# Kernel tuning notes

Hardware: AMD Instinct MI355X
Metric: run time of the kernel (lower is better)

## Reference

```python
import jax, jax.numpy as jnp
import numpy as np


def setup_inputs() -> dict:
    key = jax.random.key(0)
    B, H = 4096, 32768
    x = jax.random.normal(key, (B, H), dtype=jnp.float32)
    return {"hidden_preactivation_BH": x, "k": 64}


def reference(hidden_preactivation_BH, k):
    # top-k over last dim, then scatter values back into a zero tensor
    vals_BK, idx_BK = jax.lax.top_k(hidden_preactivation_BH, k)
    B = hidden_preactivation_BH.shape[0]
    rows_B1 = jnp.arange(B)[:, None]
    hidden_BH = jnp.zeros_like(hidden_preactivation_BH)
    hidden_BH = hidden_BH.at[rows_B1, idx_BK].set(vals_BK)
    return hidden_BH
```

## Files before the change

### kernel.cpp

```cpp
#include <hip/hip_runtime.h>
#include <stdint.h>


#define H_DIM    32768
#define NTHREADS 1024
#define VPT      (H_DIM / NTHREADS / 4)
#define CAP      2048
#define NBINS    4096

__device__ __forceinline__ uint32_t f2mono(float f) {
    uint32_t u = __float_as_uint(f);
    return (u & 0x80000000u) ? ~u : (u | 0x80000000u);
}
__device__ __forceinline__ float mono2f(uint32_t m) {
    uint32_t u = (m & 0x80000000u) ? (m & 0x7fffffffu) : ~m;
    return __uint_as_float(u);
}

__global__ __launch_bounds__(NTHREADS)
void topk_kernel(const float* __restrict__ in, const int* __restrict__ kp,
                 float* __restrict__ out)
{
    __shared__ uint32_t hist[NBINS];
    __shared__ uint32_t wave_exc[16];
    __shared__ uint32_t s_b, s_g, s_cnt;
    __shared__ uint32_t s_ncand;
    __shared__ uint32_t cand_u[CAP];
    __shared__ uint32_t cand_i[CAP];

    const uint32_t t   = threadIdx.x;
    const uint32_t row = blockIdx.x;
    const uint32_t k   = (uint32_t)kp[0];

    const float4* __restrict__ rin  = (const float4*)(in  + (size_t)row * H_DIM);
    float4*       __restrict__ rout = (float4*)(out + (size_t)row * H_DIM);

    #pragma unroll
    for (int i = 0; i < NBINS / NTHREADS; ++i) hist[t + i * NTHREADS] = 0;
    if (t == 0) s_ncand = 0;
    __syncthreads();

    uint32_t um[VPT][4];
    #pragma unroll
    for (int it = 0; it < VPT; ++it) {
        float4 v = rin[t + it * NTHREADS];
        um[it][0] = f2mono(v.x);
        um[it][1] = f2mono(v.y);
        um[it][2] = f2mono(v.z);
        um[it][3] = f2mono(v.w);
        atomicAdd(&hist[um[it][0] >> 20], 1u);
        atomicAdd(&hist[um[it][1] >> 20], 1u);
        atomicAdd(&hist[um[it][2] >> 20], 1u);
        atomicAdd(&hist[um[it][3] >> 20], 1u);
    }
    __syncthreads();

    {
        uint32_t h0 = hist[4*t], h1 = hist[4*t+1], h2 = hist[4*t+2], h3 = hist[4*t+3];
        uint32_t s = h0 + h1 + h2 + h3;
        uint32_t lane = t & 63, wid = t >> 6;
        uint32_t v = s;
        #pragma unroll
        for (int off = 1; off < 64; off <<= 1) {
            uint32_t o = __shfl_down(v, off);
            if (lane + off < 64) v += o;
        }
        if (lane == 0) wave_exc[wid] = v;
        __syncthreads();
        if (t == 0) {
            uint32_t acc = 0;
            for (int w = 15; w >= 0; --w) { uint32_t tw = wave_exc[w]; wave_exc[w] = acc; acc += tw; }
        }
        __syncthreads();
        uint32_t cumIncl = v + wave_exc[wid];
        uint32_t Ech = cumIncl - s;
        if (Ech < k && k <= Ech + s) {
            uint32_t gl = Ech;
            #pragma unroll
            for (int bb = 3; bb >= 0; --bb) {
                uint32_t h = hist[4*t + bb];
                if (gl + h >= k) { s_b = 4*t + (uint32_t)bb; s_g = gl; s_cnt = h; break; }
                gl += h;
            }
        }
    }
    __syncthreads();

    uint32_t prefix = s_b;
    uint32_t g      = s_g;
    uint32_t cnt    = s_cnt;
    uint32_t shift  = 20;

    while (cnt > CAP && shift > 0) {
        uint32_t nshift = (shift >= 12) ? (shift - 12) : 0;
        uint32_t nbits  = shift - nshift;
        uint32_t nbins  = 1u << nbits;
        __syncthreads();
        for (uint32_t i = t; i < nbins; i += NTHREADS) hist[i] = 0;
        __syncthreads();
        #pragma unroll
        for (int it = 0; it < VPT; ++it) {
            #pragma unroll
            for (int c = 0; c < 4; ++c) {
                uint32_t u = um[it][c];
                if ((u >> shift) == prefix)
                    atomicAdd(&hist[(u >> nshift) & (nbins - 1)], 1u);
            }
        }
        __syncthreads();
        if (t == 0) {
            uint32_t gl = g;
            for (int bb = (int)nbins - 1; bb >= 0; --bb) {
                uint32_t h = hist[bb];
                if (gl + h >= k) { s_b = (uint32_t)bb; s_g = gl; s_cnt = h; break; }
                gl += h;
            }
        }
        __syncthreads();
        prefix = (prefix << nbits) | s_b;
        g = s_g; cnt = s_cnt; shift = nshift;
    }

    const uint32_t need = k - g;
    #pragma unroll
    for (int it = 0; it < VPT; ++it) {
        float4 o;
        float* oc = (float*)&o;
        #pragma unroll
        for (int c = 0; c < 4; ++c) {
            uint32_t u  = um[it][c];
            uint32_t hi = u >> shift;
            float val = 0.0f;
            if (hi > prefix) {
                val = mono2f(u);
            } else if (hi == prefix) {
                uint32_t p = atomicAdd(&s_ncand, 1u);
                if (p < CAP) { cand_u[p] = u; cand_i[p] = (t + (uint32_t)it * NTHREADS) * 4u + (uint32_t)c; }
            }
            oc[c] = val;
        }
        rout[t + it * NTHREADS] = o;
    }
    __syncthreads();

    uint32_t nc = s_ncand; if (nc > CAP) nc = CAP;
    for (uint32_t i = t; i < nc; i += NTHREADS) {
        uint32_t ui = cand_u[i], ii = cand_i[i];
        uint32_t rank = 0;
        for (uint32_t j = 0; j < nc; ++j) {
            uint32_t uj = cand_u[j];
            rank += (uj > ui || (uj == ui && cand_i[j] < ii)) ? 1u : 0u;
        }
        if (rank < need) out[(size_t)row * H_DIM + ii] = mono2f(ui);
    }
}

extern "C" void kernel_launch(void* const* d_in, const int* in_sizes, int n_in,
                              void* d_out, int out_size, void* d_ws, size_t ws_size,
                              hipStream_t stream)
{
    const float* x  = (const float*)d_in[0];
    const int*   kp = (const int*)d_in[1];
    float* out = (float*)d_out;
    const int B = in_sizes[0] / H_DIM;
    hipLaunchKernelGGL(topk_kernel, dim3(B), dim3(NTHREADS), 0, stream, x, kp, out);
}
```

Baseline: 232.9 us.

## Use persistent blocks with next-row prefetch, bitmap candidate select, nontemporal IO

Launches a fixed grid of 256 persistent blocks that loop over rows, prefetching the next row into registers while the current row is processed. Selected boundary candidates are recorded in a shared bitmap so the output is written once with coalesced nontemporal stores, replacing scattered single-element writes after the main store. It also adds raw s_barrier sync and nontemporal loads. The cost is higher register pressure from the prefetch buffer, and a 256-block grid may underfill the GPU compared with one block per row.

```diff
diff --git a/kernel.cpp b/kernel.cpp
--- a/kernel.cpp
+++ b/kernel.cpp
@@ -7,6 +7,9 @@
 #define VPT      (H_DIM / NTHREADS / 4)
 #define CAP      2048
 #define NBINS    4096
+#define NWORDS   (H_DIM / 32)
+
+typedef float f32x4 __attribute__((ext_vector_type(4)));
 
 __device__ __forceinline__ uint32_t f2mono(float f) {
     uint32_t u = __float_as_uint(f);
@@ -17,141 +20,190 @@
     return __uint_as_float(u);
 }
 
-__global__ __launch_bounds__(NTHREADS)
+__device__ __forceinline__ void BAR() {
+    asm volatile("s_waitcnt lgkmcnt(0)" ::: "memory");
+    __builtin_amdgcn_s_barrier();
+}
+
+__global__ __launch_bounds__(NTHREADS, 4)
 void topk_kernel(const float* __restrict__ in, const int* __restrict__ kp,
-                 float* __restrict__ out)
+                 float* __restrict__ out, int B)
 {
     __shared__ uint32_t hist[NBINS];
+    __shared__ uint32_t bitmap[NWORDS];
     __shared__ uint32_t wave_exc[16];
     __shared__ uint32_t s_b, s_g, s_cnt;
     __shared__ uint32_t s_ncand;
     __shared__ uint32_t cand_u[CAP];
     __shared__ uint32_t cand_i[CAP];
 
-    const uint32_t t   = threadIdx.x;
-    const uint32_t row = blockIdx.x;
-    const uint32_t k   = (uint32_t)kp[0];
-
-    const float4* __restrict__ rin  = (const float4*)(in  + (size_t)row * H_DIM);
-    float4*       __restrict__ rout = (float4*)(out + (size_t)row * H_DIM);
-
-    #pragma unroll
-    for (int i = 0; i < NBINS / NTHREADS; ++i) hist[t + i * NTHREADS] = 0;
-    if (t == 0) s_ncand = 0;
-    __syncthreads();
-
-    uint32_t um[VPT][4];
-    #pragma unroll
-    for (int it = 0; it < VPT; ++it) {
-        float4 v = rin[t + it * NTHREADS];
-        um[it][0] = f2mono(v.x);
-        um[it][1] = f2mono(v.y);
-        um[it][2] = f2mono(v.z);
-        um[it][3] = f2mono(v.w);
-        atomicAdd(&hist[um[it][0] >> 20], 1u);
-        atomicAdd(&hist[um[it][1] >> 20], 1u);
-        atomicAdd(&hist[um[it][2] >> 20], 1u);
-        atomicAdd(&hist[um[it][3] >> 20], 1u);
+    const uint32_t t = threadIdx.x;
+    const uint32_t k = (uint32_t)kp[0];
+
+    int row = (int)blockIdx.x;
+    const int rstride = (int)gridDim.x;
+
+    f32x4 buf[VPT];
+    if (row < B) {
+        const f32x4* __restrict__ rin = (const f32x4*)(in + (size_t)row * H_DIM);
+        #pragma unroll
+        for (int i = 0; i < VPT; ++i)
+            buf[i] = __builtin_nontemporal_load(&rin[t + i * NTHREADS]);
     }
-    __syncthreads();
-
-    {
-        uint32_t h0 = hist[4*t], h1 = hist[4*t+1], h2 = hist[4*t+2], h3 = hist[4*t+3];
-        uint32_t s = h0 + h1 + h2 + h3;
-        uint32_t lane = t & 63, wid = t >> 6;
-        uint32_t v = s;
-        #pragma unroll
-        for (int off = 1; off < 64; off <<= 1) {
-            uint32_t o = __shfl_down(v, off);
-            if (lane + off < 64) v += o;
-        }
-        if (lane == 0) wave_exc[wid] = v;
-        __syncthreads();
-        if (t == 0) {
-            uint32_t acc = 0;
-            for (int w = 15; w >= 0; --w) { uint32_t tw = wave_exc[w]; wave_exc[w] = acc; acc += tw; }
-        }
-        __syncthreads();
-        uint32_t cumIncl = v + wave_exc[wid];
-        uint32_t Ech = cumIncl - s;
-        if (Ech < k && k <= Ech + s) {
-            uint32_t gl = Ech;
-            #pragma unroll
-            for (int bb = 3; bb >= 0; --bb) {
-                uint32_t h = hist[4*t + bb];
-                if (gl + h >= k) { s_b = 4*t + (uint32_t)bb; s_g = gl; s_cnt = h; break; }
-                gl += h;
-            }
-        }
-    }
-    __syncthreads();
-
-    uint32_t prefix = s_b;
-    uint32_t g      = s_g;
-    uint32_t cnt    = s_cnt;
-    uint32_t shift  = 20;
-
-    while (cnt > CAP && shift > 0) {
-        uint32_t nshift = (shift >= 12) ? (shift - 12) : 0;
-        uint32_t nbits  = shift - nshift;
-        uint32_t nbins  = 1u << nbits;
-        __syncthreads();
-        for (uint32_t i = t; i < nbins; i += NTHREADS) hist[i] = 0;
-        __syncthreads();
+
+    for (; row < B; row += rstride) {
+        uint32_t um[VPT][4];
+        #pragma unroll
+        for (int i = 0; i < VPT; ++i) {
+            um[i][0] = f2mono(buf[i].x);
+            um[i][1] = f2mono(buf[i].y);
+            um[i][2] = f2mono(buf[i].z);
+            um[i][3] = f2mono(buf[i].w);
+        }
+        {
+            int nr = row + rstride;
+            if (nr < B) {
+                const f32x4* __restrict__ rin = (const f32x4*)(in + (size_t)nr * H_DIM);
+                #pragma unroll
+                for (int i = 0; i < VPT; ++i)
+                    buf[i] = __builtin_nontemporal_load(&rin[t + i * NTHREADS]);
+            }
+        }
+
+        BAR();
+        #pragma unroll
+        for (int i = 0; i < NBINS / NTHREADS; ++i) hist[t + i * NTHREADS] = 0;
+        bitmap[t] = 0;
+        if (t == 0) s_ncand = 0;
+        BAR();
+
+        #pragma unroll
+        for (int it = 0; it < VPT; ++it) {
+            atomicAdd(&hist[um[it][0] >> 20], 1u);
+            atomicAdd(&hist[um[it][1] >> 20], 1u);
+            atomicAdd(&hist[um[it][2] >> 20], 1u);
+            atomicAdd(&hist[um[it][3] >> 20], 1u);
+        }
+        BAR();
+
+        {
+            uint32_t h0 = hist[4*t], h1 = hist[4*t+1], h2 = hist[4*t+2], h3 = hist[4*t+3];
+            uint32_t s = h0 + h1 + h2 + h3;
+            uint32_t lane = t & 63, wid = t >> 6;
+            uint32_t v = s;
+            #pragma unroll
+            for (int off = 1; off < 64; off <<= 1) {
+                uint32_t o = __shfl_down(v, off);
+                if (lane + off < 64) v += o;
+            }
+            if (lane == 0) wave_exc[wid] = v;
+            BAR();
+            if (t == 0) {
+                uint32_t acc = 0;
+                for (int w = 15; w >= 0; --w) { uint32_t tw = wave_exc[w]; wave_exc[w] = acc; acc += tw; }
+            }
+            BAR();
+            uint32_t cumIncl = v + wave_exc[wid];
+            uint32_t Ech = cumIncl - s;
+            if (Ech < k && k <= Ech + s) {
+                uint32_t gl = Ech;
+                #pragma unroll
+                for (int bb = 3; bb >= 0; --bb) {
+                    uint32_t h = hist[4*t + bb];
+                    if (gl + h >= k) { s_b = 4*t + (uint32_t)bb; s_g = gl; s_cnt = h; break; }
+                    gl += h;
+                }
+            }
+        }
+        BAR();
+
+        uint32_t prefix = s_b;
+        uint32_t g      = s_g;
+        uint32_t cnt    = s_cnt;
+        uint32_t shift  = 20;
+
+        while (cnt > CAP && shift > 0) {
+            uint32_t nshift = (shift >= 12) ? (shift - 12) : 0;
+            uint32_t nbits  = shift - nshift;
+            uint32_t nbins  = 1u << nbits;
+            BAR();
+            for (uint32_t i = t; i < nbins; i += NTHREADS) hist[i] = 0;
+            BAR();
+            #pragma unroll
+            for (int it = 0; it < VPT; ++it) {
+                #pragma unroll
+                for (int c = 0; c < 4; ++c) {
+                    uint32_t u = um[it][c];
+                    if ((u >> shift) == prefix)
+                        atomicAdd(&hist[(u >> nshift) & (nbins - 1)], 1u);
+                }
+            }
+            BAR();
+            if (t == 0) {
+                uint32_t gl = g;
+                for (int bb = (int)nbins - 1; bb >= 0; --bb) {
+                    uint32_t h = hist[bb];
+                    if (gl + h >= k) { s_b = (uint32_t)bb; s_g = gl; s_cnt = h; break; }
+                    gl += h;
+                }
+            }
+            BAR();
+            prefix = (prefix << nbits) | s_b;
+            g = s_g; cnt = s_cnt; shift = nshift;
+        }
+
+        const uint32_t need = k - g;
         #pragma unroll
         for (int it = 0; it < VPT; ++it) {
             #pragma unroll
             for (int c = 0; c < 4; ++c) {
                 uint32_t u = um[it][c];
-                if ((u >> shift) == prefix)
-                    atomicAdd(&hist[(u >> nshift) & (nbins - 1)], 1u);
-            }
-        }
-        __syncthreads();
-        if (t == 0) {
-            uint32_t gl = g;
-            for (int bb = (int)nbins - 1; bb >= 0; --bb) {
-                uint32_t h = hist[bb];
-                if (gl + h >= k) { s_b = (uint32_t)bb; s_g = gl; s_cnt = h; break; }
-                gl += h;
-            }
-        }
-        __syncthreads();
-        prefix = (prefix << nbits) | s_b;
-        g = s_g; cnt = s_cnt; shift = nshift;
-    }
-
-    const uint32_t need = k - g;
-    #pragma unroll
-    for (int it = 0; it < VPT; ++it) {
-        float4 o;
-        float* oc = (float*)&o;
-        #pragma unroll
-        for (int c = 0; c < 4; ++c) {
-            uint32_t u  = um[it][c];
-            uint32_t hi = u >> shift;
-            float val = 0.0f;
-            if (hi > prefix) {
-                val = mono2f(u);
-            } else if (hi == prefix) {
-                uint32_t p = atomicAdd(&s_ncand, 1u);
-                if (p < CAP) { cand_u[p] = u; cand_i[p] = (t + (uint32_t)it * NTHREADS) * 4u + (uint32_t)c; }
-            }
-            oc[c] = val;
-        }
-        rout[t + it * NTHREADS] = o;
-    }
-    __syncthreads();
-
-    uint32_t nc = s_ncand; if (nc > CAP) nc = CAP;
-    for (uint32_t i = t; i < nc; i += NTHREADS) {
-        uint32_t ui = cand_u[i], ii = cand_i[i];
-        uint32_t rank = 0;
-        for (uint32_t j = 0; j < nc; ++j) {
-            uint32_t uj = cand_u[j];
-            rank += (uj > ui || (uj == ui && cand_i[j] < ii)) ? 1u : 0u;
-        }
-        if (rank < need) out[(size_t)row * H_DIM + ii] = mono2f(ui);
+                if ((u >> shift) == prefix) {
+                    uint32_t p = atomicAdd(&s_ncand, 1u);
+                    if (p < CAP) {
+                        cand_u[p] = u;
+                        cand_i[p] = (t + (uint32_t)it * NTHREADS) * 4u + (uint32_t)c;
+                    }
+                }
+            }
+        }
+        BAR();
+
+        {
+            uint32_t nc = s_ncand; if (nc > CAP) nc = CAP;
+            for (uint32_t i = t; i < nc; i += NTHREADS) {
+                uint32_t ui = cand_u[i], ii = cand_i[i];
+                uint32_t rank = 0;
+                for (uint32_t j = 0; j < nc; ++j) {
+                    uint32_t uj = cand_u[j];
+                    rank += (uj > ui || (uj == ui && cand_i[j] < ii)) ? 1u : 0u;
+                }
+                if (rank < need) atomicOr(&bitmap[ii >> 5], 1u << (ii & 31));
+            }
+        }
+        BAR();
+
+        {
+            f32x4* __restrict__ rout = (f32x4*)(out + (size_t)row * H_DIM);
+            #pragma unroll
+            for (int it = 0; it < VPT; ++it) {
+                f32x4 o;
+                #pragma unroll
+                for (int c = 0; c < 4; ++c) {
+                    uint32_t u  = um[it][c];
+                    uint32_t hi = u >> shift;
+                    float val = 0.0f;
+                    if (hi > prefix) {
+                        val = mono2f(u);
+                    } else if (hi == prefix) {
+                        uint32_t ii = (t + (uint32_t)it * NTHREADS) * 4u + (uint32_t)c;
+                        if ((bitmap[ii >> 5] >> (ii & 31)) & 1u) val = mono2f(u);
+                    }
+                    o[c] = val;
+                }
+                __builtin_nontemporal_store(o, &rout[t + it * NTHREADS]);
+            }
+        }
     }
 }
 
@@ -163,5 +215,6 @@
     const int*   kp = (const int*)d_in[1];
     float* out = (float*)d_out;
     const int B = in_sizes[0] / H_DIM;
-    hipLaunchKernelGGL(topk_kernel, dim3(B), dim3(NTHREADS), 0, stream, x, kp, out);
-}
+    int grid = B < 256 ? B : 256;
+    hipLaunchKernelGGL(topk_kernel, dim3(grid), dim3(NTHREADS), 0, stream, x, kp, out, B);
+}
```

Measured after the change: 306.5 us. 1.32x slower.
